# Kernel tuning notes

Hardware: AMD Instinct MI355X
Metric: run time of the kernel (lower is better)

## Reference

```python
import jax, jax.numpy as jnp
import numpy as np

B, C, H, W, O = 32, 512, 28, 28, 1024


def _make_sketch(key, input_dim, output_dim):
    kh, ks = jax.random.split(key)
    rand_h = jax.random.randint(kh, (input_dim,), 0, output_dim)
    rand_s = jax.random.randint(ks, (input_dim,), 0, 2).astype(jnp.float32) * 2.0 - 1.0
    sketch = jnp.zeros((output_dim, input_dim), dtype=jnp.float32)
    return sketch.at[rand_h, jnp.arange(input_dim)].set(rand_s)


def setup_inputs() -> dict:
    key = jax.random.key(0)
    k1, k2, k3, k4 = jax.random.split(key, 4)
    x1 = jax.random.normal(k1, (B, C, H, W), dtype=jnp.float32)
    x2 = jax.random.normal(k2, (B, C, H, W), dtype=jnp.float32)
    sketch1 = _make_sketch(k3, C, O)
    sketch2 = _make_sketch(k4, C, O)
    return {"x1": x1, "x2": x2, "sketch1": sketch1, "sketch2": sketch2}


def reference(x1, x2, sketch1, sketch2):
    b, c, h, w = x1.shape
    out_dim = sketch1.shape[0]
    # [B, C, H*W] -> [B, N, C]
    x1_flat = x1.reshape(b, c, h * w).transpose(0, 2, 1)
    x2_flat = x2.reshape(b, c, h * w).transpose(0, 2, 1)
    # count-sketch projection via dense matmul (faithful to F.linear)
    proj1 = jnp.einsum('bnc,oc->bno', x1_flat, sketch1)
    proj2 = jnp.einsum('bnc,oc->bno', x2_flat, sketch2)
    orig_dtype = proj1.dtype
    # circular convolution via FFT along output_dim axis
    fft1 = jnp.fft.fft(proj1.astype(jnp.float32), axis=-1)
    fft2 = jnp.fft.fft(proj2.astype(jnp.float32), axis=-1)
    cbp_flat = jnp.fft.ifft(fft1 * fft2, axis=-1).real.astype(orig_dtype)
    # [B, N, O] -> [B, O, H, W]
    return cbp_flat.transpose(0, 2, 1).reshape(b, out_dim, h, w)
```

## Files before the change

### kernel.cpp

```cpp
#include <hip/hip_runtime.h>

#define O_DIM   1024
#define C_DIM   512
#define HW      784
#define B_DIM   32
#define T_POS   4
#define NTILES  (HW / T_POS)
#define NTHREADS 128
#define NBLK    (B_DIM * NTILES)
#define RPAD    5

typedef float v2f __attribute__((ext_vector_type(2)));

__device__ __forceinline__ v2f cmul(v2f a, v2f b) {
    v2f bs = __builtin_shufflevector(b, b, 1, 0);
    v2f an = {-a.y, a.y};
    return a.x * b + an * bs;
}

static constexpr int REV5[32] = {
    0,16,8,24,4,20,12,28,2,18,10,26,6,22,14,30,
    1,17,9,25,5,21,13,29,3,19,11,27,7,23,15,31};

static constexpr float C32T[16] = {
    1.f, 0.98078528f, 0.92387953f, 0.83146961f,
    0.70710678f, 0.55557023f, 0.38268343f, 0.19509032f,
    0.f, -0.19509032f, -0.38268343f, -0.55557023f,
    -0.70710678f, -0.83146961f, -0.92387953f, -0.98078528f};
static constexpr float S32T[16] = {
    0.f, 0.19509032f, 0.38268343f, 0.55557023f,
    0.70710678f, 0.83146961f, 0.92387953f, 0.98078528f,
    1.f, 0.98078528f, 0.92387953f, 0.83146961f,
    0.70710678f, 0.55557023f, 0.38268343f, 0.19509032f};

__device__ __forceinline__ void fft32f(v2f y[32]) {
#pragma unroll
    for (int s = 0; s < 5; ++s) {
        const int L = 32 >> s;
        const int h = 16 >> s;
#pragma unroll
        for (int u = 0; u < 16; ++u) {
            const int blk = u >> (4 - s);
            const int t   = u & (h - 1);
            const int i   = blk * L + t;
            const int m   = t << s;
            v2f a = y[i], b = y[i + h];
            y[i] = a + b;
            v2f d = a - b;
            if (m == 0) {
                y[i + h] = d;
            } else if (m == 8) {
                y[i + h] = (v2f){d.y, -d.x};
            } else {
                y[i + h] = cmul(d, (v2f){C32T[m], -S32T[m]});
            }
        }
    }
}

__device__ __forceinline__ void four_step_Bf(v2f* zg, int p, v2f y[32]) {
    float sv, cv;
    __sincosf(-6.283185307179586f * (float)p * (1.f / 1024.f), &sv, &cv);
    const v2f stw = {cv, sv};
    v2f t2  = cmul(stw, stw);
    v2f t4  = cmul(t2, t2);
    v2f s8  = cmul(t4, t4);
    v2f s16 = cmul(s8, s8);
    v2f s24 = cmul(s16, s8);
    v2f wq0 = {1.f, 0.f}, wq1 = s8, wq2 = s16, wq3 = s24;
#pragma unroll
    for (int m = 0; m < 8; ++m) {
        {   const int k2 = m;
            v2f val = y[REV5[k2]];
            if (k2 > 0) val = cmul(val, wq0);
            zg[k2 * 32 + ((p + k2) & 31)] = val; }
        {   const int k2 = 8 + m;
            zg[k2 * 32 + ((p + k2) & 31)] = cmul(y[REV5[k2]], wq1); }
        {   const int k2 = 16 + m;
            zg[k2 * 32 + ((p + k2) & 31)] = cmul(y[REV5[k2]], wq2); }
        {   const int k2 = 24 + m;
            zg[k2 * 32 + ((p + k2) & 31)] = cmul(y[REV5[k2]], wq3); }
        if (m < 7) {
            wq0 = cmul(wq0, stw); wq1 = cmul(wq1, stw);
            wq2 = cmul(wq2, stw); wq3 = cmul(wq3, stw);
        }
    }
    __builtin_amdgcn_wave_barrier();
#pragma unroll
    for (int n1 = 0; n1 < 32; ++n1)
        y[n1] = zg[p * 32 + ((n1 + p) & 31)];
    __builtin_amdgcn_wave_barrier();
    fft32f(y);
}

__global__ void extract_sketch(const float* __restrict__ sk1,
                               const float* __restrict__ sk2,
                               int* __restrict__ h, float* __restrict__ s) {
    const int o = blockIdx.x;
    for (int c = threadIdx.x; c < C_DIM; c += blockDim.x) {
        float v1 = sk1[o * C_DIM + c];
        if (v1 != 0.f) { h[c] = o; s[c] = v1; }
        float v2 = sk2[o * C_DIM + c];
        if (v2 != 0.f) { h[C_DIM + c] = o; s[C_DIM + c] = v2; }
    }
}

__global__ __launch_bounds__(NTHREADS, 2)
void cbp_main(const float* __restrict__ x1, const float* __restrict__ x2,
              const int* __restrict__ h1, const int* __restrict__ h2,
              const float* __restrict__ s1, const float* __restrict__ s2,
              float* __restrict__ out) {
    __shared__ float4 LBUF[2048];
    float* Zs = reinterpret_cast<float*>(LBUF);
    float* R  = reinterpret_cast<float*>(LBUF);

    const int tid = threadIdx.x;
    const int wid  = blockIdx.x;
    const int work = (wid & 7) * (NBLK >> 3) + (wid >> 3);
    const int b    = work / NTILES;
    const int tile = work % NTILES;
    const int n0   = tile * T_POS;

    const int xoff = b * (C_DIM * HW) + n0;
    float4 xa[4], xb[4];
    int    qa[4], qb[4];
    float  wa[4], wb[4];
#pragma unroll
    for (int r = 0; r < 4; ++r) {
        const int c = tid + NTHREADS * r;
        xa[r] = *(const float4*)(x1 + xoff + c * HW);
        xb[r] = *(const float4*)(x2 + xoff + c * HW);
        qa[r] = h1[c];  qb[r] = h2[c];
        wa[r] = s1[c];  wb[r] = s2[c];
    }

#pragma unroll
    for (int i = 0; i < 2048 / NTHREADS; ++i)
        LBUF[tid + NTHREADS * i] = make_float4(0.f, 0.f, 0.f, 0.f);
    __syncthreads();

#pragma unroll
    for (int r = 0; r < 4; ++r) {
        float va[4] = {xa[r].x, xa[r].y, xa[r].z, xa[r].w};
#pragma unroll
        for (int j = 0; j < 4; ++j)
            __hip_atomic_fetch_add(&Zs[(j * O_DIM + qa[r]) * 2 + 0],
                                   wa[r] * va[j],
                                   __ATOMIC_RELAXED, __HIP_MEMORY_SCOPE_WORKGROUP);
        float vb[4] = {xb[r].x, xb[r].y, xb[r].z, xb[r].w};
#pragma unroll
        for (int j = 0; j < 4; ++j)
            __hip_atomic_fetch_add(&Zs[(j * O_DIM + qb[r]) * 2 + 1],
                                   wb[r] * vb[j],
                                   __ATOMIC_RELAXED, __HIP_MEMORY_SCOPE_WORKGROUP);
    }
    __syncthreads();

    const int g    = tid >> 5;
    const int p    = tid & 31;
    const int lane = tid & 63;
    v2f* zg = reinterpret_cast<v2f*>(LBUF) + g * O_DIM;
    const int paddr = (((lane & 32) | ((32 - p) & 31))) << 2;

    v2f y[32];

#pragma unroll 1
    for (int iter = 0; iter < 2; ++iter) {
        if (iter == 0) {
#pragma unroll
            for (int n2 = 0; n2 < 32; ++n2)
                y[n2] = zg[p + 32 * n2];
            __builtin_amdgcn_wave_barrier();
        } else {
            v2f t[32];
#pragma unroll
            for (int n2 = 0; n2 < 32; ++n2) {
                v2f za = y[REV5[n2]];
                v2f yb = y[REV5[31 - n2]];
                v2f zb;
                zb.x = __uint_as_float((unsigned)__builtin_amdgcn_ds_bpermute(
                           paddr, (int)__float_as_uint(yb.x)));
                zb.y = __uint_as_float((unsigned)__builtin_amdgcn_ds_bpermute(
                           paddr, (int)__float_as_uint(yb.y)));
                v2f self = y[REV5[(32 - n2) & 31]];
                zb.x = (p == 0) ? self.x : zb.x;
                zb.y = (p == 0) ? self.y : zb.y;
                v2f F1c = { za.x + zb.x, zb.y - za.y };
                v2f F2c = { za.y + zb.y, za.x - zb.x };
                t[n2] = cmul(F1c, F2c);
            }
#pragma unroll
            for (int i = 0; i < 32; ++i) y[i] = t[i];
        }
        fft32f(y);
        four_step_Bf(zg, p, y);
    }
    __syncthreads();

#pragma unroll
    for (int k1 = 0; k1 < 32; ++k1)
        R[(p + 32 * k1) * RPAD + g] = y[REV5[k1]].x * (0.25f / 1024.f);
    __syncthreads();

    const int obase = b * (O_DIM * HW) + n0;
#pragma unroll
    for (int r = 0; r < O_DIM / NTHREADS; ++r) {
        const int o = tid + NTHREADS * r;
        const float* rp = &R[o * RPAD];
        float4 v0 = make_float4(rp[0], rp[1], rp[2], rp[3]);
        *(float4*)(out + obase + o * HW) = v0;
    }
}

extern "C" void kernel_launch(void* const* d_in, const int* in_sizes, int n_in,
                              void* d_out, int out_size, void* d_ws, size_t ws_size,
                              hipStream_t stream) {
    const float* x1  = (const float*)d_in[0];
    const float* x2  = (const float*)d_in[1];
    const float* sk1 = (const float*)d_in[2];
    const float* sk2 = (const float*)d_in[3];
    float* out = (float*)d_out;

    int*   h = (int*)d_ws;
    float* s = (float*)((char*)d_ws + 4096);

    hipLaunchKernelGGL(extract_sketch, dim3(O_DIM), dim3(256), 0, stream,
                       sk1, sk2, h, s);
    hipLaunchKernelGGL(cbp_main, dim3(NBLK), dim3(NTHREADS), 0, stream,
                       x1, x2, h, h + C_DIM, s, s + C_DIM, out);
}
```

Before: 353.6 us.

## Split each 1024-point FFT across two half-waves using cross-lane butterflies

Each 1024-point complex FFT was previously handled by 32 lanes holding 32 values each. It is now spread over 64 lanes holding 16 values each, with the first radix-2 stage exchanged across half-waves via ds_bpermute. Block size doubles to 256 threads and the occupancy hint rises to 4, with the second transform using a DIT variant so it ends in a layout the output stage can use. The aim is lower register pressure and more latency hiding, at the cost of extra cross-lane permutes, select logic and more complex index bookkeeping.

After: 348.4 us. No clear change (-1.5%).

```diff
diff --git a/kernel.cpp b/kernel.cpp
--- a/kernel.cpp
+++ b/kernel.cpp
@@ -6,7 +6,7 @@
 #define B_DIM   32
 #define T_POS   4
 #define NTILES  (HW / T_POS)
-#define NTHREADS 128
+#define NTHREADS 256
 #define NBLK    (B_DIM * NTILES)
 #define RPAD    5
 
@@ -18,9 +18,17 @@
     return a.x * b + an * bs;
 }
 
-static constexpr int REV5[32] = {
-    0,16,8,24,4,20,12,28,2,18,10,26,6,22,14,30,
-    1,17,9,25,5,21,13,29,3,19,11,27,7,23,15,31};
+__device__ __forceinline__ v2f bperm(int addr, v2f v) {
+    v2f r;
+    r.x = __uint_as_float((unsigned)__builtin_amdgcn_ds_bpermute(
+              addr, (int)__float_as_uint(v.x)));
+    r.y = __uint_as_float((unsigned)__builtin_amdgcn_ds_bpermute(
+              addr, (int)__float_as_uint(v.y)));
+    return r;
+}
+
+static constexpr int REV4[16] = {0,8,4,12,2,10,6,14,1,9,5,13,3,11,7,15};
+static constexpr int J0A[16]  = {0,1,3,2,7,6,5,4,15,14,13,12,11,10,9,8};
 
 static constexpr float C32T[16] = {
     1.f, 0.98078528f, 0.92387953f, 0.83146961f,
@@ -33,64 +41,72 @@
     1.f, 0.98078528f, 0.92387953f, 0.83146961f,
     0.70710678f, 0.55557023f, 0.38268343f, 0.19509032f};
 
-__device__ __forceinline__ void fft32f(v2f y[32]) {
-#pragma unroll
-    for (int s = 0; s < 5; ++s) {
-        const int L = 32 >> s;
-        const int h = 16 >> s;
-#pragma unroll
-        for (int u = 0; u < 16; ++u) {
-            const int blk = u >> (4 - s);
-            const int t   = u & (h - 1);
+__device__ __forceinline__ void fft32x(v2f y[16], int h, int xaddr) {
+#pragma unroll
+    for (int j = 0; j < 16; ++j) {
+        v2f own = y[j];
+        v2f oth = bperm(xaddr, own);
+        v2f sum = own + oth;
+        v2f f   = own - oth;
+        v2f dd;
+        if (j == 0)      dd = -f;
+        else if (j == 8) dd = (v2f){-f.y, f.x};
+        else             dd = cmul(f, (v2f){-C32T[j], S32T[j]});
+        y[j].x = h ? dd.x : sum.x;
+        y[j].y = h ? dd.y : sum.y;
+    }
+#pragma unroll
+    for (int s = 0; s < 4; ++s) {
+        const int hh = 8 >> s;
+        const int L  = 16 >> s;
+#pragma unroll
+        for (int u = 0; u < 8; ++u) {
+            const int blk = u >> (3 - s);
+            const int t   = u & (hh - 1);
             const int i   = blk * L + t;
-            const int m   = t << s;
-            v2f a = y[i], b = y[i + h];
+            const int m   = (t << s) * 2;
+            v2f a = y[i], b = y[i + hh];
             y[i] = a + b;
             v2f d = a - b;
-            if (m == 0) {
-                y[i + h] = d;
-            } else if (m == 8) {
-                y[i + h] = (v2f){d.y, -d.x};
-            } else {
-                y[i + h] = cmul(d, (v2f){C32T[m], -S32T[m]});
-            }
-        }
-    }
-}
-
-__device__ __forceinline__ void four_step_Bf(v2f* zg, int p, v2f y[32]) {
-    float sv, cv;
-    __sincosf(-6.283185307179586f * (float)p * (1.f / 1024.f), &sv, &cv);
-    const v2f stw = {cv, sv};
-    v2f t2  = cmul(stw, stw);
-    v2f t4  = cmul(t2, t2);
-    v2f s8  = cmul(t4, t4);
-    v2f s16 = cmul(s8, s8);
-    v2f s24 = cmul(s16, s8);
-    v2f wq0 = {1.f, 0.f}, wq1 = s8, wq2 = s16, wq3 = s24;
-#pragma unroll
-    for (int m = 0; m < 8; ++m) {
-        {   const int k2 = m;
-            v2f val = y[REV5[k2]];
-            if (k2 > 0) val = cmul(val, wq0);
-            zg[k2 * 32 + ((p + k2) & 31)] = val; }
-        {   const int k2 = 8 + m;
-            zg[k2 * 32 + ((p + k2) & 31)] = cmul(y[REV5[k2]], wq1); }
-        {   const int k2 = 16 + m;
-            zg[k2 * 32 + ((p + k2) & 31)] = cmul(y[REV5[k2]], wq2); }
-        {   const int k2 = 24 + m;
-            zg[k2 * 32 + ((p + k2) & 31)] = cmul(y[REV5[k2]], wq3); }
-        if (m < 7) {
-            wq0 = cmul(wq0, stw); wq1 = cmul(wq1, stw);
-            wq2 = cmul(wq2, stw); wq3 = cmul(wq3, stw);
-        }
-    }
-    __builtin_amdgcn_wave_barrier();
-#pragma unroll
-    for (int n1 = 0; n1 < 32; ++n1)
-        y[n1] = zg[p * 32 + ((n1 + p) & 31)];
-    __builtin_amdgcn_wave_barrier();
-    fft32f(y);
+            if (m == 0)      y[i + hh] = d;
+            else if (m == 8) y[i + hh] = (v2f){d.y, -d.x};
+            else             y[i + hh] = cmul(d, (v2f){C32T[m], -S32T[m]});
+        }
+    }
+}
+
+__device__ __forceinline__ void fft32x_dit(v2f y[16], int h, int xaddr) {
+#pragma unroll
+    for (int s = 0; s < 4; ++s) {
+        const int half = 1 << s;
+        const int lowmask = half - 1;
+#pragma unroll
+        for (int u = 0; u < 8; ++u) {
+            const int i = ((u & ~lowmask) << 1) | (u & lowmask);
+            const int m = (i & lowmask) * (16 >> s);
+            v2f a = y[i], b = y[i + half];
+            v2f t;
+            if (m == 0)      t = b;
+            else if (m == 8) t = (v2f){b.y, -b.x};
+            else             t = cmul(b, (v2f){C32T[m], -S32T[m]});
+            y[i]        = a + t;
+            y[i + half] = a - t;
+        }
+    }
+#pragma unroll
+    for (int j = 0; j < 16; ++j) {
+        v2f own = y[j];
+        v2f oth = bperm(xaddr, own);
+        v2f aa, bb;
+        aa.x = h ? oth.x : own.x;  aa.y = h ? oth.y : own.y;
+        bb.x = h ? own.x : oth.x;  bb.y = h ? own.y : oth.y;
+        v2f t;
+        if (j == 0)      t = bb;
+        else if (j == 8) t = (v2f){bb.y, -bb.x};
+        else             t = cmul(bb, (v2f){C32T[j], -S32T[j]});
+        y[j].x = h ? aa.x - t.x : aa.x + t.x;
+        y[j].y = h ? aa.y - t.y : aa.y + t.y;
+    }
 }
 
 __global__ void extract_sketch(const float* __restrict__ sk1,
@@ -105,7 +121,7 @@
     }
 }
 
-__global__ __launch_bounds__(NTHREADS, 2)
+__global__ __launch_bounds__(NTHREADS, 4)
 void cbp_main(const float* __restrict__ x1, const float* __restrict__ x2,
               const int* __restrict__ h1, const int* __restrict__ h2,
               const float* __restrict__ s1, const float* __restrict__ s2,
@@ -121,85 +137,160 @@
     const int tile = work % NTILES;
     const int n0   = tile * T_POS;
 
+    const int c0 = tid;
+    const int c1 = tid + NTHREADS;
     const int xoff = b * (C_DIM * HW) + n0;
-    float4 xa[4], xb[4];
-    int    qa[4], qb[4];
-    float  wa[4], wb[4];
-#pragma unroll
-    for (int r = 0; r < 4; ++r) {
-        const int c = tid + NTHREADS * r;
-        xa[r] = *(const float4*)(x1 + xoff + c * HW);
-        xb[r] = *(const float4*)(x2 + xoff + c * HW);
-        qa[r] = h1[c];  qb[r] = h2[c];
-        wa[r] = s1[c];  wb[r] = s2[c];
-    }
+    float4 xa0 = *(const float4*)(x1 + xoff + c0 * HW);
+    float4 xa1 = *(const float4*)(x1 + xoff + c1 * HW);
+    float4 xb0 = *(const float4*)(x2 + xoff + c0 * HW);
+    float4 xb1 = *(const float4*)(x2 + xoff + c1 * HW);
+    const int   q10 = h1[c0], q11 = h1[c1], q20 = h2[c0], q21 = h2[c1];
+    const float w10 = s1[c0], w11 = s1[c1], w20 = s2[c0], w21 = s2[c1];
 
 #pragma unroll
     for (int i = 0; i < 2048 / NTHREADS; ++i)
         LBUF[tid + NTHREADS * i] = make_float4(0.f, 0.f, 0.f, 0.f);
     __syncthreads();
 
-#pragma unroll
-    for (int r = 0; r < 4; ++r) {
-        float va[4] = {xa[r].x, xa[r].y, xa[r].z, xa[r].w};
+    {
+        float va[4] = {xa0.x, xa0.y, xa0.z, xa0.w};
 #pragma unroll
         for (int j = 0; j < 4; ++j)
-            __hip_atomic_fetch_add(&Zs[(j * O_DIM + qa[r]) * 2 + 0],
-                                   wa[r] * va[j],
+            __hip_atomic_fetch_add(&Zs[(j * O_DIM + q10) * 2 + 0], w10 * va[j],
                                    __ATOMIC_RELAXED, __HIP_MEMORY_SCOPE_WORKGROUP);
-        float vb[4] = {xb[r].x, xb[r].y, xb[r].z, xb[r].w};
+        float vb[4] = {xa1.x, xa1.y, xa1.z, xa1.w};
 #pragma unroll
         for (int j = 0; j < 4; ++j)
-            __hip_atomic_fetch_add(&Zs[(j * O_DIM + qb[r]) * 2 + 1],
-                                   wb[r] * vb[j],
+            __hip_atomic_fetch_add(&Zs[(j * O_DIM + q11) * 2 + 0], w11 * vb[j],
                                    __ATOMIC_RELAXED, __HIP_MEMORY_SCOPE_WORKGROUP);
+        float vc[4] = {xb0.x, xb0.y, xb0.z, xb0.w};
+#pragma unroll
+        for (int j = 0; j < 4; ++j)
+            __hip_atomic_fetch_add(&Zs[(j * O_DIM + q20) * 2 + 1], w20 * vc[j],
+                                   __ATOMIC_RELAXED, __HIP_MEMORY_SCOPE_WORKGROUP);
+        float vd[4] = {xb1.x, xb1.y, xb1.z, xb1.w};
+#pragma unroll
+        for (int j = 0; j < 4; ++j)
+            __hip_atomic_fetch_add(&Zs[(j * O_DIM + q21) * 2 + 1], w21 * vd[j],
+                                   __ATOMIC_RELAXED, __HIP_MEMORY_SCOPE_WORKGROUP);
     }
     __syncthreads();
 
-    const int g    = tid >> 5;
-    const int p    = tid & 31;
+    const int wv   = tid >> 6;
     const int lane = tid & 63;
-    v2f* zg = reinterpret_cast<v2f*>(LBUF) + g * O_DIM;
-    const int paddr = (((lane & 32) | ((32 - p) & 31))) << 2;
-
-    v2f y[32];
-
-#pragma unroll 1
-    for (int iter = 0; iter < 2; ++iter) {
-        if (iter == 0) {
-#pragma unroll
-            for (int n2 = 0; n2 < 32; ++n2)
-                y[n2] = zg[p + 32 * n2];
-            __builtin_amdgcn_wave_barrier();
-        } else {
-            v2f t[32];
-#pragma unroll
-            for (int n2 = 0; n2 < 32; ++n2) {
-                v2f za = y[REV5[n2]];
-                v2f yb = y[REV5[31 - n2]];
-                v2f zb;
-                zb.x = __uint_as_float((unsigned)__builtin_amdgcn_ds_bpermute(
-                           paddr, (int)__float_as_uint(yb.x)));
-                zb.y = __uint_as_float((unsigned)__builtin_amdgcn_ds_bpermute(
-                           paddr, (int)__float_as_uint(yb.y)));
-                v2f self = y[REV5[(32 - n2) & 31]];
-                zb.x = (p == 0) ? self.x : zb.x;
-                zb.y = (p == 0) ? self.y : zb.y;
-                v2f F1c = { za.x + zb.x, zb.y - za.y };
-                v2f F2c = { za.y + zb.y, za.x - zb.x };
-                t[n2] = cmul(F1c, F2c);
+    const int c    = lane & 31;
+    const int h    = lane >> 5;
+    v2f* zg = reinterpret_cast<v2f*>(LBUF) + wv * O_DIM;
+    const int xaddr = (lane ^ 32) << 2;
+    const int paddr = ((((32 - c) & 31) | ((1 - h) << 5)) << 2);
+
+    float sv, cv;
+    __sincosf(-6.283185307179586f * (float)c * (1.f / 1024.f), &sv, &cv);
+    const v2f cs = {cv, sv};
+
+    v2f y[16];
+
+#pragma unroll
+    for (int j = 0; j < 16; ++j)
+        y[j] = zg[c + 32 * (16 * h + j)];
+    __builtin_amdgcn_wave_barrier();
+    fft32x(y, h, xaddr);
+
+    {
+        v2f step  = cmul(cs, cs);
+        v2f st2   = cmul(step, step);
+        v2f st4   = cmul(st2, st2);
+        v2f st8   = cmul(st4, st4);
+        v2f st12  = cmul(st8, st4);
+        v2f base;
+        base.x = h ? cs.x : 1.f;
+        base.y = h ? cs.y : 0.f;
+        v2f w0 = base, w1 = cmul(base, st4), w2 = cmul(base, st8),
+            w3 = cmul(base, st12);
+#pragma unroll
+        for (int mm = 0; mm < 4; ++mm) {
+            {   const int m = mm;          const int k2 = 2 * m + h;
+                zg[k2 * 32 + ((c + k2) & 31)] = cmul(y[REV4[m]], w0); }
+            {   const int m = 4 + mm;      const int k2 = 2 * m + h;
+                zg[k2 * 32 + ((c + k2) & 31)] = cmul(y[REV4[m]], w1); }
+            {   const int m = 8 + mm;      const int k2 = 2 * m + h;
+                zg[k2 * 32 + ((c + k2) & 31)] = cmul(y[REV4[m]], w2); }
+            {   const int m = 12 + mm;     const int k2 = 2 * m + h;
+                zg[k2 * 32 + ((c + k2) & 31)] = cmul(y[REV4[m]], w3); }
+            if (mm < 3) {
+                w0 = cmul(w0, step); w1 = cmul(w1, step);
+                w2 = cmul(w2, step); w3 = cmul(w3, step);
             }
-#pragma unroll
-            for (int i = 0; i < 32; ++i) y[i] = t[i];
-        }
-        fft32f(y);
-        four_step_Bf(zg, p, y);
-    }
+        }
+    }
+    __builtin_amdgcn_wave_barrier();
+#pragma unroll
+    for (int j = 0; j < 16; ++j)
+        y[j] = zg[c * 32 + ((16 * h + j + c) & 31)];
+    __builtin_amdgcn_wave_barrier();
+    fft32x(y, h, xaddr);
+
+    {
+        v2f t[16];
+#pragma unroll
+        for (int j = 0; j < 16; ++j) {
+            v2f za   = y[j];
+            v2f push = y[15 - j];
+            v2f zb   = bperm(paddr, push);
+            v2f selfA = y[J0A[j]];
+            v2f self;
+            self.x = h ? push.x : selfA.x;
+            self.y = h ? push.y : selfA.y;
+            zb.x = (c == 0) ? self.x : zb.x;
+            zb.y = (c == 0) ? self.y : zb.y;
+            v2f F1c = { za.x + zb.x, zb.y - za.y };
+            v2f F2c = { za.y + zb.y, za.x - zb.x };
+            t[j] = cmul(F1c, F2c);
+        }
+#pragma unroll
+        for (int j = 0; j < 16; ++j) y[j] = t[j];
+    }
+
+    fft32x_dit(y, h, xaddr);
+
+    {
+        v2f cs2  = cmul(cs, cs);
+        v2f cs4  = cmul(cs2, cs2);
+        v2f cs8  = cmul(cs4, cs4);
+        v2f cs12 = cmul(cs8, cs4);
+        v2f cs16 = cmul(cs8, cs8);
+        v2f base;
+        base.x = h ? cs16.x : 1.f;
+        base.y = h ? cs16.y : 0.f;
+        v2f w0 = base, w1 = cmul(base, cs4), w2 = cmul(base, cs8),
+            w3 = cmul(base, cs12);
+#pragma unroll
+        for (int mm = 0; mm < 4; ++mm) {
+            {   const int j = mm;          const int k2 = 16 * h + j;
+                zg[k2 * 32 + ((c + k2) & 31)] = cmul(y[j], w0); }
+            {   const int j = 4 + mm;      const int k2 = 16 * h + j;
+                zg[k2 * 32 + ((c + k2) & 31)] = cmul(y[j], w1); }
+            {   const int j = 8 + mm;      const int k2 = 16 * h + j;
+                zg[k2 * 32 + ((c + k2) & 31)] = cmul(y[j], w2); }
+            {   const int j = 12 + mm;     const int k2 = 16 * h + j;
+                zg[k2 * 32 + ((c + k2) & 31)] = cmul(y[j], w3); }
+            if (mm < 3) {
+                w0 = cmul(w0, cs); w1 = cmul(w1, cs);
+                w2 = cmul(w2, cs); w3 = cmul(w3, cs);
+            }
+        }
+    }
+    __builtin_amdgcn_wave_barrier();
+#pragma unroll
+    for (int j = 0; j < 16; ++j)
+        y[j] = zg[c * 32 + ((16 * h + j + c) & 31)];
+    __builtin_amdgcn_wave_barrier();
+    fft32x(y, h, xaddr);
     __syncthreads();
 
 #pragma unroll
-    for (int k1 = 0; k1 < 32; ++k1)
-        R[(p + 32 * k1) * RPAD + g] = y[REV5[k1]].x * (0.25f / 1024.f);
+    for (int j = 0; j < 16; ++j)
+        R[(c + 32 * (2 * REV4[j] + h)) * RPAD + wv] = y[j].x * (0.25f / 1024.f);
     __syncthreads();
 
     const int obase = b * (O_DIM * HW) + n0;
```
